# Performance work log

Measured on AMD Instinct MI355X. Metric: run time of the kernel, lower is better.

Reference implementation:

```python
import jax, jax.numpy as jnp
import numpy as np

NUM_HEAD = 16
DIM_HEAD = 64
SCALE = DIM_HEAD ** -0.5


def setup_inputs() -> dict:
    key = jax.random.key(0)
    k1, k2, k3 = jax.random.split(key, 3)
    B, N, D = 4, 2048, 1024
    x = jax.random.normal(k1, (B, N, D), dtype=jnp.float32)
    w_qkv = jax.random.normal(k2, (D, 3 * NUM_HEAD * DIM_HEAD), dtype=jnp.float32) * (D ** -0.5)
    w_out = jax.random.normal(k3, (NUM_HEAD * DIM_HEAD, D), dtype=jnp.float32) * ((NUM_HEAD * DIM_HEAD) ** -0.5)
    return {"x": x, "w_qkv": w_qkv, "w_out": w_out}


def reference(x, w_qkv, w_out):
    B, N, D = x.shape
    qkv = x @ w_qkv  # [B, N, 3*H*Dh]
    q, k, v = jnp.split(qkv, 3, axis=-1)
    def heads(t):
        return t.reshape(B, N, NUM_HEAD, DIM_HEAD).transpose(0, 2, 1, 3)  # b h n d
    q, k, v = heads(q), heads(k), heads(v)
    scores = jnp.einsum('bhnd,bhmd->bhnm', q, k) * SCALE
    attn = jax.nn.softmax(scores, axis=-1)
    out = jnp.einsum('bhnm,bhmd->bhnd', attn, v)
    out = out.transpose(0, 2, 1, 3).reshape(B, N, NUM_HEAD * DIM_HEAD)
    return out @ w_out
```

## Files before the change

kernel.cpp:

```cpp
#include <hip/hip_runtime.h>
#include <hip/hip_bf16.h>
#include <stdint.h>


typedef __attribute__((ext_vector_type(8))) __bf16 bf16x8;
typedef __attribute__((ext_vector_type(4))) __bf16 bf16x4;
typedef __attribute__((ext_vector_type(4))) float f32x4;
typedef __attribute__((ext_vector_type(16))) float f32x16;
typedef __attribute__((ext_vector_type(4))) unsigned int u32x4;

#define EXPC 0.18033688011112042f
#define MC2 32.0f

static __device__ __forceinline__ void gload_lds16(const void* g, void* s) {
  __builtin_amdgcn_global_load_lds(
      (__attribute__((address_space(1))) unsigned int*)g,
      (__attribute__((address_space(3))) unsigned int*)s, 16, 0, 0);
}

__global__ void k_cvt(const float* __restrict__ src, __bf16* __restrict__ dst, int n4) {
  int i = blockIdx.x * blockDim.x + threadIdx.x;
  if (i >= n4) return;
  float4 v = reinterpret_cast<const float4*>(src)[i];
  bf16x4 o = { (__bf16)v.x, (__bf16)v.y, (__bf16)v.z, (__bf16)v.w };
  *reinterpret_cast<bf16x4*>(dst + (size_t)i * 4) = o;
}

__global__ void k_tcvt(const float* __restrict__ src, __bf16* __restrict__ dst, int W, int Hs) {
  __shared__ float tile[32][33];
  int tx = threadIdx.x, ty = threadIdx.y;
  int x = blockIdx.x * 32 + tx;
  int y0 = blockIdx.y * 32;
  for (int j = ty; j < 32; j += 8) tile[j][tx] = src[(size_t)(y0 + j) * W + x];
  __syncthreads();
  int xo = y0 + tx;
  int yo = blockIdx.x * 32;
  for (int j = ty; j < 32; j += 8) dst[(size_t)(yo + j) * Hs + xo] = (__bf16)tile[tx][j];
}

static __device__ __forceinline__ void gemm_core(
    const __bf16* __restrict__ A, const __bf16* __restrict__ BT, int K,
    int m0, int n0, f32x4 acc[4][4], __bf16* As, __bf16* Bs) {
  const int tid = threadIdx.x;
  const int lane = tid & 63, w = tid >> 6;
  const int fr = lane & 15, fq = lane >> 4;
  const int srow = lane >> 2, scol = (lane & 3) * 8;
  const int wr = (w >> 1) * 64, wc = (w & 1) * 64;
#pragma unroll
  for (int mi = 0; mi < 4; ++mi)
#pragma unroll
    for (int nj = 0; nj < 4; ++nj) acc[mi][nj] = (f32x4){0.f, 0.f, 0.f, 0.f};

  for (int ko = 0; ko < K; ko += 32) {
#pragma unroll
    for (int i = 0; i < 2; ++i) {
      int rb = w * 32 + i * 16;
      gload_lds16(A + (size_t)(m0 + rb + srow) * K + ko + scol, As + rb * 32);
      gload_lds16(BT + (size_t)(n0 + rb + srow) * K + ko + scol, Bs + rb * 32);
    }
    __syncthreads();
    bf16x8 af[4], bfv[4];
#pragma unroll
    for (int mi = 0; mi < 4; ++mi)
      af[mi] = *(const bf16x8*)(As + (wr + mi * 16 + fr) * 32 + fq * 8);
#pragma unroll
    for (int nj = 0; nj < 4; ++nj)
      bfv[nj] = *(const bf16x8*)(Bs + (wc + nj * 16 + fr) * 32 + fq * 8);
#pragma unroll
    for (int mi = 0; mi < 4; ++mi)
#pragma unroll
      for (int nj = 0; nj < 4; ++nj)
        acc[mi][nj] = __builtin_amdgcn_mfma_f32_16x16x32_bf16(af[mi], bfv[nj], acc[mi][nj], 0, 0, 0);
    __syncthreads();
  }
}

__global__ __launch_bounds__(256) void k_gemm_qkv(
    const __bf16* __restrict__ A, const __bf16* __restrict__ BT,
    __bf16* __restrict__ qb, __bf16* __restrict__ kb, __bf16* __restrict__ vb) {
  __shared__ __align__(16) __bf16 As[128 * 32];
  __shared__ __align__(16) __bf16 Bs[128 * 32];
  f32x4 acc[4][4];
  int m0 = blockIdx.x * 128, n0 = blockIdx.y * 128;
  gemm_core(A, BT, 1024, m0, n0, acc, As, Bs);
  const int lane = threadIdx.x & 63, w = threadIdx.x >> 6;
  const int fr = lane & 15, fq = lane >> 4;
  const int wr = (w >> 1) * 64, wc = (w & 1) * 64;
  const int which = n0 >> 10;
#pragma unroll
  for (int mi = 0; mi < 4; ++mi) {
#pragma unroll
    for (int nj = 0; nj < 4; ++nj) {
      int row = m0 + wr + mi * 16 + fq * 4;
      int col = n0 + wc + nj * 16 + fr;
      int rem = col & 1023, h = rem >> 6, d = rem & 63;
      int bb = row >> 11, n = row & 2047;
      int bh = bb * 16 + h;
      if (which == 2) {
        bf16x4 pk = { (__bf16)acc[mi][nj][0], (__bf16)acc[mi][nj][1],
                      (__bf16)acc[mi][nj][2], (__bf16)acc[mi][nj][3] };
        *reinterpret_cast<bf16x4*>(vb + ((size_t)bh * 64 + d) * 2048 + n) = pk;
      } else {
        __bf16* dst = (which == 0) ? qb : kb;
#pragma unroll
        for (int j = 0; j < 4; ++j)
          dst[((size_t)bh * 2048 + (n + j)) * 64 + d] = (__bf16)acc[mi][nj][j];
      }
    }
  }
}

__global__ __launch_bounds__(256) void k_gemm_out(
    const __bf16* __restrict__ A, const __bf16* __restrict__ BT, float* __restrict__ C) {
  __shared__ __align__(16) __bf16 As[128 * 32];
  __shared__ __align__(16) __bf16 Bs[128 * 32];
  f32x4 acc[4][4];
  int m0 = blockIdx.x * 128, n0 = blockIdx.y * 128;
  gemm_core(A, BT, 1024, m0, n0, acc, As, Bs);
  const int lane = threadIdx.x & 63, w = threadIdx.x >> 6;
  const int fr = lane & 15, fq = lane >> 4;
  const int wr = (w >> 1) * 64, wc = (w & 1) * 64;
#pragma unroll
  for (int mi = 0; mi < 4; ++mi)
#pragma unroll
    for (int nj = 0; nj < 4; ++nj)
#pragma unroll
      for (int j = 0; j < 4; ++j)
        C[(size_t)(m0 + wr + mi * 16 + fq * 4 + j) * 1024 + n0 + wc + nj * 16 + fr] =
            acc[mi][nj][j];
}

__global__ __launch_bounds__(256, 4) void k_attn(
    const __bf16* __restrict__ qb, const __bf16* __restrict__ kb,
    const __bf16* __restrict__ vb, __bf16* __restrict__ ao) {
  __shared__ __align__(16) __bf16 Ks[2][64 * 64];
  __shared__ __align__(16) __bf16 Vs[2][64 * 64];
  const int tid = threadIdx.x, lane = tid & 63, wid = tid >> 6;
  const int r31 = lane & 31, hi = lane >> 5;
  const int lsw = (lane & 7) ^ ((lane >> 3) & 3);
  const int bh = blockIdx.x & 63, qblk = blockIdx.x >> 6;
  const __bf16* kbase = kb + (size_t)bh * 2048 * 64;
  const __bf16* vbase = vb + (size_t)bh * 64 * 2048;

  const int nbase = qblk * 128 + wid * 32;
  const __bf16* qptr = qb + ((size_t)bh * 2048 + nbase + r31) * 64;
  bf16x8 qf[4];
#pragma unroll
  for (int dd = 0; dd < 4; ++dd)
    qf[dd] = *(const bf16x8*)(qptr + dd * 16 + hi * 8);

  f32x16 o0, o1;
#pragma unroll
  for (int r = 0; r < 16; ++r) { o0[r] = 0.f; o1[r] = 0.f; }
  float lsum = 0.f;

  auto stage = [&](int buf, int j0) {
#pragma unroll
    for (int p2 = 0; p2 < 2; ++p2) {
      int row = p2 * 32 + (tid >> 3);
      int sc = (tid & 7) ^ (row & 7) ^ ((row >> 3) & 3);
      int dst = p2 * 2048 + wid * 512;
      gload_lds16(kbase + (size_t)(j0 + row) * 64 + sc * 8, &Ks[buf][dst]);
      gload_lds16(vbase + (size_t)row * 2048 + j0 + sc * 8, &Vs[buf][dst]);
    }
  };

  stage(0, 0);
  __syncthreads();

  for (int kt = 0; kt < 32; ++kt) {
    const int cur = kt & 1;
    if (kt < 31) stage(cur ^ 1, (kt + 1) * 64);

#pragma unroll
    for (int h2 = 0; h2 < 2; ++h2) {
      const int kro = h2 * 32;

      f32x16 sa;
#pragma unroll
      for (int r = 0; r < 16; ++r) sa[r] = 0.f;
      __builtin_amdgcn_s_setprio(1);
#pragma unroll
      for (int dd = 0; dd < 4; ++dd) {
        bf16x8 kf = *(const bf16x8*)(&Ks[cur][(kro + r31) * 64 + (((dd * 2 + hi) ^ lsw) << 3)]);
        sa = __builtin_amdgcn_mfma_f32_32x32x16_bf16(kf, qf[dd], sa, 0, 0, 0);
      }
      __builtin_amdgcn_s_setprio(0);

      float rs0 = 0.f, rs1 = 0.f;
      unsigned pw[8];
#pragma unroll
      for (int r = 0; r < 8; ++r) {
        float e0 = __builtin_amdgcn_exp2f(fmaf(sa[2 * r], EXPC, -MC2));
        float e1 = __builtin_amdgcn_exp2f(fmaf(sa[2 * r + 1], EXPC, -MC2));
        rs0 += e0; rs1 += e1;
        asm("v_cvt_pk_bf16_f32 %0, %1, %2" : "=v"(pw[r]) : "v"(e0), "v"(e1));
      }
      lsum += rs0 + rs1;

      __builtin_amdgcn_s_setprio(1);
#define PVSTEP(W0, W1, W2, W3, KK) do {                                              \
        unsigned a0 = (W0), a1 = (W1), b0 = (W2), b1 = (W3);                         \
        asm("v_permlane32_swap_b32 %0, %1" : "+v"(a0), "+v"(b0));                    \
        asm("v_permlane32_swap_b32 %0, %1" : "+v"(a1), "+v"(b1));                    \
        u32x4 fw = {a0, a1, b0, b1};                                                 \
        bf16x8 pa = __builtin_bit_cast(bf16x8, fw);                                  \
        bf16x8 v0 = *(const bf16x8*)(&Vs[cur][r31 * 64 + ((((KK) * 2 + hi) ^ lsw) << 3)]); \
        bf16x8 v1 = *(const bf16x8*)(&Vs[cur][(32 + r31) * 64 + ((((KK) * 2 + hi) ^ lsw) << 3)]); \
        o0 = __builtin_amdgcn_mfma_f32_32x32x16_bf16(pa, v0, o0, 0, 0, 0);           \
        o1 = __builtin_amdgcn_mfma_f32_32x32x16_bf16(pa, v1, o1, 0, 0, 0);           \
      } while (0)
      PVSTEP(pw[0], pw[1], pw[2], pw[3], 2 * h2);
      PVSTEP(pw[4], pw[5], pw[6], pw[7], 2 * h2 + 1);
#undef PVSTEP
      __builtin_amdgcn_s_setprio(0);
    }

    __syncthreads();
  }

  lsum += __shfl_xor(lsum, 32, 64);
  float inv = 1.0f / lsum;
  const int b = bh >> 4, h = bh & 15;
  __bf16* abase = ao + ((size_t)b * 2048 + nbase) * 1024 + h * 64 + r31;
#pragma unroll
  for (int r = 0; r < 16; ++r) {
    int qrow = (r & 3) + 8 * (r >> 2) + 4 * hi;
    float ir = __shfl(inv, qrow, 64);
    abase[(size_t)qrow * 1024] = (__bf16)(o0[r] * ir);
    abase[(size_t)qrow * 1024 + 32] = (__bf16)(o1[r] * ir);
  }
}

extern "C" void kernel_launch(void* const* d_in, const int* in_sizes, int n_in,
                              void* d_out, int out_size, void* d_ws, size_t ws_size,
                              hipStream_t stream) {
  (void)in_sizes; (void)n_in; (void)out_size; (void)ws_size;
  const float* x = (const float*)d_in[0];
  const float* w_qkv = (const float*)d_in[1];
  const float* w_out = (const float*)d_in[2];
  float* out = (float*)d_out;

  char* p = (char*)d_ws;
  __bf16* xb    = (__bf16*)p; p += (size_t)8192 * 1024 * 2;
  __bf16* wqkvT = (__bf16*)p; p += (size_t)3072 * 1024 * 2;
  __bf16* woutT = (__bf16*)p; p += (size_t)1024 * 1024 * 2;
  __bf16* qb    = (__bf16*)p; p += (size_t)64 * 2048 * 64 * 2;
  __bf16* kb    = (__bf16*)p; p += (size_t)64 * 2048 * 64 * 2;
  __bf16* vb    = (__bf16*)p; p += (size_t)64 * 64 * 2048 * 2;
  __bf16* ao    = (__bf16*)p; p += (size_t)8192 * 1024 * 2;

  k_cvt<<<8192, 256, 0, stream>>>(x, xb, 2097152);
  k_tcvt<<<dim3(96, 32), dim3(32, 8), 0, stream>>>(w_qkv, wqkvT, 3072, 1024);
  k_tcvt<<<dim3(32, 32), dim3(32, 8), 0, stream>>>(w_out, woutT, 1024, 1024);
  k_gemm_qkv<<<dim3(64, 24), 256, 0, stream>>>(xb, wqkvT, qb, kb, vb);
  k_attn<<<dim3(1024), dim3(256), 0, stream>>>(qb, kb, vb, ao);
  k_gemm_out<<<dim3(64, 8), 256, 0, stream>>>(ao, woutT, out);
}
```

Before: 196.0 us.

## Replace GEMM core with 256x256 double-buffered swizzled LDS pipeline

Both projection GEMMs now use 256x256 tiles with 512 threads, where each wave computes a 128x64 sub-tile over K-steps of 64. Two LDS stages are filled with async global-to-LDS loads, and the next stage's loads are interleaved with MFMA work under manual waitcnt and barrier control plus setprio hints. An XOR swizzle on the LDS chunks is meant to avoid bank conflicts. The goal is more data reuse per tile and overlap of memory with compute. The trade-offs are a much larger LDS footprint and fewer blocks (only 128 for the output GEMM), which may leave CUs idle.

```diff
diff --git a/kernel.cpp b/kernel.cpp
--- a/kernel.cpp
+++ b/kernel.cpp
@@ -38,61 +38,122 @@
   for (int j = ty; j < 32; j += 8) dst[(size_t)(yo + j) * Hs + xo] = (__bf16)tile[tx][j];
 }
 
-static __device__ __forceinline__ void gemm_core(
+static __device__ __forceinline__ void gemm256_core8(
     const __bf16* __restrict__ A, const __bf16* __restrict__ BT, int K,
-    int m0, int n0, f32x4 acc[4][4], __bf16* As, __bf16* Bs) {
+    int m0, int n0, f32x4 acc[8][4], __bf16* S) {
   const int tid = threadIdx.x;
-  const int lane = tid & 63, w = tid >> 6;
+  const int lane = tid & 63, wid = tid >> 6;
   const int fr = lane & 15, fq = lane >> 4;
-  const int srow = lane >> 2, scol = (lane & 3) * 8;
-  const int wr = (w >> 1) * 64, wc = (w & 1) * 64;
-#pragma unroll
-  for (int mi = 0; mi < 4; ++mi)
+  const int fr7 = fr & 7;
+  const int wm = wid >> 2, wn = wid & 3;
+  const int srow = tid >> 3;
+  const int schunk = (tid & 7) ^ (srow & 7);
+  const int NT = K >> 6;
+
+#pragma unroll
+  for (int mi = 0; mi < 8; ++mi)
 #pragma unroll
     for (int nj = 0; nj < 4; ++nj) acc[mi][nj] = (f32x4){0.f, 0.f, 0.f, 0.f};
 
-  for (int ko = 0; ko < K; ko += 32) {
-#pragma unroll
-    for (int i = 0; i < 2; ++i) {
-      int rb = w * 32 + i * 16;
-      gload_lds16(A + (size_t)(m0 + rb + srow) * K + ko + scol, As + rb * 32);
-      gload_lds16(BT + (size_t)(n0 + rb + srow) * K + ko + scol, Bs + rb * 32);
+  auto stage_panel = [&](int buf, int kt, int which) {
+    const __bf16* G = which ? BT : A;
+    const int base0 = which ? n0 : m0;
+    __bf16* L = S + buf * 32768 + which * 16384 + wid * 512;
+#pragma unroll
+    for (int i = 0; i < 4; ++i)
+      gload_lds16(G + (size_t)(base0 + i * 64 + srow) * K + kt * 64 + schunk * 8,
+                  L + i * 4096);
+  };
+
+  stage_panel(0, 0, 0); stage_panel(0, 0, 1);
+  stage_panel(1, 1, 0); stage_panel(1, 1, 1);
+  asm volatile("s_waitcnt vmcnt(8)" ::: "memory");
+  __builtin_amdgcn_s_barrier();
+  __builtin_amdgcn_sched_barrier(0);
+
+  for (int kt = 0; kt < NT; ++kt) {
+    const int c = kt & 1;
+    const __bf16* Sa = S + c * 32768;
+    const __bf16* Sb = Sa + 16384;
+    bf16x8 af0[8], bf0[4], af1[8], bf1[4];
+
+#pragma unroll
+    for (int mi = 0; mi < 8; ++mi)
+      af0[mi] = *(const bf16x8*)(Sa + (wm * 128 + mi * 16 + fr) * 64 + ((fq ^ fr7) << 3));
+#pragma unroll
+    for (int nj = 0; nj < 4; ++nj)
+      bf0[nj] = *(const bf16x8*)(Sb + (wn * 64 + nj * 16 + fr) * 64 + ((fq ^ fr7) << 3));
+    asm volatile("s_waitcnt lgkmcnt(0)" ::: "memory");
+    __builtin_amdgcn_sched_barrier(0);
+    __builtin_amdgcn_s_setprio(1);
+#pragma unroll
+    for (int mi = 0; mi < 8; ++mi)
+#pragma unroll
+      for (int nj = 0; nj < 2; ++nj)
+        acc[mi][nj] = __builtin_amdgcn_mfma_f32_16x16x32_bf16(af0[mi], bf0[nj], acc[mi][nj], 0, 0, 0);
+    __builtin_amdgcn_s_setprio(0);
+
+#pragma unroll
+    for (int mi = 0; mi < 8; ++mi)
+      af1[mi] = *(const bf16x8*)(Sa + (wm * 128 + mi * 16 + fr) * 64 + (((4 + fq) ^ fr7) << 3));
+#pragma unroll
+    for (int nj = 0; nj < 4; ++nj)
+      bf1[nj] = *(const bf16x8*)(Sb + (wn * 64 + nj * 16 + fr) * 64 + (((4 + fq) ^ fr7) << 3));
+    __builtin_amdgcn_s_setprio(1);
+#pragma unroll
+    for (int mi = 0; mi < 8; ++mi)
+#pragma unroll
+      for (int nj = 2; nj < 4; ++nj)
+        acc[mi][nj] = __builtin_amdgcn_mfma_f32_16x16x32_bf16(af0[mi], bf0[nj], acc[mi][nj], 0, 0, 0);
+    __builtin_amdgcn_s_setprio(0);
+    asm volatile("s_waitcnt lgkmcnt(0)" ::: "memory");
+    __builtin_amdgcn_s_barrier();
+    __builtin_amdgcn_sched_barrier(0);
+
+    if (kt + 2 < NT) stage_panel(c, kt + 2, 0);
+    __builtin_amdgcn_s_setprio(1);
+#pragma unroll
+    for (int mi = 0; mi < 8; ++mi)
+#pragma unroll
+      for (int nj = 0; nj < 2; ++nj)
+        acc[mi][nj] = __builtin_amdgcn_mfma_f32_16x16x32_bf16(af1[mi], bf1[nj], acc[mi][nj], 0, 0, 0);
+    __builtin_amdgcn_s_setprio(0);
+
+    if (kt + 2 < NT) stage_panel(c, kt + 2, 1);
+    __builtin_amdgcn_s_setprio(1);
+#pragma unroll
+    for (int mi = 0; mi < 8; ++mi)
+#pragma unroll
+      for (int nj = 2; nj < 4; ++nj)
+        acc[mi][nj] = __builtin_amdgcn_mfma_f32_16x16x32_bf16(af1[mi], bf1[nj], acc[mi][nj], 0, 0, 0);
+    __builtin_amdgcn_s_setprio(0);
+
+    if (kt < NT - 1) {
+      if (kt + 2 < NT) asm volatile("s_waitcnt vmcnt(8)" ::: "memory");
+      else             asm volatile("s_waitcnt vmcnt(0)" ::: "memory");
+      __builtin_amdgcn_s_barrier();
+      __builtin_amdgcn_sched_barrier(0);
     }
-    __syncthreads();
-    bf16x8 af[4], bfv[4];
-#pragma unroll
-    for (int mi = 0; mi < 4; ++mi)
-      af[mi] = *(const bf16x8*)(As + (wr + mi * 16 + fr) * 32 + fq * 8);
-#pragma unroll
-    for (int nj = 0; nj < 4; ++nj)
-      bfv[nj] = *(const bf16x8*)(Bs + (wc + nj * 16 + fr) * 32 + fq * 8);
-#pragma unroll
-    for (int mi = 0; mi < 4; ++mi)
-#pragma unroll
-      for (int nj = 0; nj < 4; ++nj)
-        acc[mi][nj] = __builtin_amdgcn_mfma_f32_16x16x32_bf16(af[mi], bfv[nj], acc[mi][nj], 0, 0, 0);
-    __syncthreads();
   }
 }
 
-__global__ __launch_bounds__(256) void k_gemm_qkv(
+__global__ __launch_bounds__(512, 2) void k_gemm_qkv(
     const __bf16* __restrict__ A, const __bf16* __restrict__ BT,
     __bf16* __restrict__ qb, __bf16* __restrict__ kb, __bf16* __restrict__ vb) {
-  __shared__ __align__(16) __bf16 As[128 * 32];
-  __shared__ __align__(16) __bf16 Bs[128 * 32];
-  f32x4 acc[4][4];
-  int m0 = blockIdx.x * 128, n0 = blockIdx.y * 128;
-  gemm_core(A, BT, 1024, m0, n0, acc, As, Bs);
-  const int lane = threadIdx.x & 63, w = threadIdx.x >> 6;
+  __shared__ __align__(16) __bf16 S[2 * 32768];
+  f32x4 acc[8][4];
+  int m0 = blockIdx.x * 256, n0 = blockIdx.y * 256;
+  gemm256_core8(A, BT, 1024, m0, n0, acc, S);
+  const int lane = threadIdx.x & 63, wid = threadIdx.x >> 6;
   const int fr = lane & 15, fq = lane >> 4;
-  const int wr = (w >> 1) * 64, wc = (w & 1) * 64;
+  const int wm = wid >> 2, wn = wid & 3;
   const int which = n0 >> 10;
 #pragma unroll
-  for (int mi = 0; mi < 4; ++mi) {
+  for (int mi = 0; mi < 8; ++mi) {
 #pragma unroll
     for (int nj = 0; nj < 4; ++nj) {
-      int row = m0 + wr + mi * 16 + fq * 4;
-      int col = n0 + wc + nj * 16 + fr;
+      int row = m0 + wm * 128 + mi * 16 + fq * 4;
+      int col = n0 + wn * 64 + nj * 16 + fr;
       int rem = col & 1023, h = rem >> 6, d = rem & 63;
       int bb = row >> 11, n = row & 2047;
       int bh = bb * 16 + h;
@@ -110,23 +171,22 @@
   }
 }
 
-__global__ __launch_bounds__(256) void k_gemm_out(
+__global__ __launch_bounds__(512, 2) void k_gemm_out(
     const __bf16* __restrict__ A, const __bf16* __restrict__ BT, float* __restrict__ C) {
-  __shared__ __align__(16) __bf16 As[128 * 32];
-  __shared__ __align__(16) __bf16 Bs[128 * 32];
-  f32x4 acc[4][4];
-  int m0 = blockIdx.x * 128, n0 = blockIdx.y * 128;
-  gemm_core(A, BT, 1024, m0, n0, acc, As, Bs);
-  const int lane = threadIdx.x & 63, w = threadIdx.x >> 6;
+  __shared__ __align__(16) __bf16 S[2 * 32768];
+  f32x4 acc[8][4];
+  int m0 = blockIdx.x * 256, n0 = blockIdx.y * 256;
+  gemm256_core8(A, BT, 1024, m0, n0, acc, S);
+  const int lane = threadIdx.x & 63, wid = threadIdx.x >> 6;
   const int fr = lane & 15, fq = lane >> 4;
-  const int wr = (w >> 1) * 64, wc = (w & 1) * 64;
-#pragma unroll
-  for (int mi = 0; mi < 4; ++mi)
+  const int wm = wid >> 2, wn = wid & 3;
+#pragma unroll
+  for (int mi = 0; mi < 8; ++mi)
 #pragma unroll
     for (int nj = 0; nj < 4; ++nj)
 #pragma unroll
       for (int j = 0; j < 4; ++j)
-        C[(size_t)(m0 + wr + mi * 16 + fq * 4 + j) * 1024 + n0 + wc + nj * 16 + fr] =
+        C[(size_t)(m0 + wm * 128 + mi * 16 + fq * 4 + j) * 1024 + n0 + wn * 64 + nj * 16 + fr] =
             acc[mi][nj][j];
 }
 
@@ -253,7 +313,7 @@
   k_cvt<<<8192, 256, 0, stream>>>(x, xb, 2097152);
   k_tcvt<<<dim3(96, 32), dim3(32, 8), 0, stream>>>(w_qkv, wqkvT, 3072, 1024);
   k_tcvt<<<dim3(32, 32), dim3(32, 8), 0, stream>>>(w_out, woutT, 1024, 1024);
-  k_gemm_qkv<<<dim3(64, 24), 256, 0, stream>>>(xb, wqkvT, qb, kb, vb);
+  k_gemm_qkv<<<dim3(32, 12), 512, 0, stream>>>(xb, wqkvT, qb, kb, vb);
   k_attn<<<dim3(1024), dim3(256), 0, stream>>>(qb, kb, vb, ao);
-  k_gemm_out<<<dim3(64, 8), 256, 0, stream>>>(ao, woutT, out);
-}
+  k_gemm_out<<<dim3(32, 4), 512, 0, stream>>>(ao, woutT, out);
+}
```

Measured after the change: 193.5 us. About the same (-1.3%).
